# Performance work log

Hardware: AMD Instinct MI355X
Metric: run time of the kernel (lower is better)

Reference implementation:

```python
import jax, jax.numpy as jnp
import numpy as np

TREE = 128
BASIC = 128
EPS = 1e-5


def layer_norm(x, g, b):
    m = jnp.mean(x, axis=-1, keepdims=True)
    v = jnp.mean((x - m) ** 2, axis=-1, keepdims=True)
    return (x - m) * jax.lax.rsqrt(v + EPS) * g + b


def setup_inputs() -> dict:
    key = jax.random.key(0)
    ks = jax.random.split(key, 32)
    n2, n1, n0 = 320000, 80000, 20000
    inp = {
        'subtree_h_top': jax.random.normal(ks[0], (n2, TREE), jnp.float32),
        'atom_x_1': jax.random.normal(ks[1], (n1, BASIC), jnp.float32),
        'atom_x_0': jax.random.normal(ks[2], (n0, BASIC), jnp.float32),
        'bond_x_2': jax.random.normal(ks[3], (n2, BASIC), jnp.float32),
        'bond_x_1': jax.random.normal(ks[4], (n1, BASIC), jnp.float32),
        'branch_W1': jax.random.normal(ks[5], (2, TREE + BASIC, TREE), jnp.float32) * 0.05,
        'branch_b1': jnp.zeros((2, TREE), jnp.float32),
        'branch_g1': jnp.ones((2, TREE), jnp.float32),
        'branch_beta1': jnp.zeros((2, TREE), jnp.float32),
        'branch_W2': jax.random.normal(ks[6], (2, TREE, TREE), jnp.float32) * 0.05,
        'branch_b2': jnp.zeros((2, TREE), jnp.float32),
        'branch_g2': jnp.ones((2, TREE), jnp.float32),
        'branch_beta2': jnp.zeros((2, TREE), jnp.float32),
        'sub_W1': jax.random.normal(ks[7], (2, BASIC + TREE, TREE), jnp.float32) * 0.05,
        'sub_b1': jnp.zeros((2, TREE), jnp.float32),
        'sub_g1': jnp.ones((2, TREE), jnp.float32),
        'sub_beta1': jnp.zeros((2, TREE), jnp.float32),
        'sub_W2': jax.random.normal(ks[8], (2, TREE, TREE), jnp.float32) * 0.05,
        'sub_b2': jnp.zeros((2, TREE), jnp.float32),
        'sub_g2': jnp.ones((2, TREE), jnp.float32),
        'sub_beta2': jnp.zeros((2, TREE), jnp.float32),
        'head_W': jax.random.normal(ks[9], (2, BASIC + TREE, TREE), jnp.float32) * 0.05,
        'head_b': jnp.zeros((2, TREE), jnp.float32),
        'head_g': jnp.ones((2, TREE), jnp.float32),
        'head_beta': jnp.zeros((2, TREE), jnp.float32),
        'src_2': jax.random.randint(ks[10], (n2,), 0, n2),
        'dst_2': jax.random.randint(ks[11], (n2,), 0, n1),
        'src_1': jax.random.randint(ks[12], (n1,), 0, n1),
        'dst_1': jax.random.randint(ks[13], (n1,), 0, n0),
    }
    return inp


def reference(subtree_h_top, atom_x_1, atom_x_0, bond_x_2, bond_x_1,
              branch_W1, branch_b1, branch_g1, branch_beta1,
              branch_W2, branch_b2, branch_g2, branch_beta2,
              sub_W1, sub_b1, sub_g1, sub_beta1,
              sub_W2, sub_b2, sub_g2, sub_beta2,
              head_W, head_b, head_g, head_beta,
              src_2, dst_2, src_1, dst_1):
    relu = jax.nn.relu
    h = subtree_h_top  # subtree_h of level tree_level nodes
    atom_xs = (atom_x_1, atom_x_0)
    bond_xs = (bond_x_2, bond_x_1)
    srcs = (src_2, src_1)
    dsts = (dst_2, dst_1)
    for i in range(2):  # i=0 -> k=2, i=1 -> k=1 (fixed small loop over tree levels)
        ax = atom_xs[i]
        # Branch_Update: edge MLP on [subtree_h[src], bond_x]
        ex = jnp.concatenate([h[srcs[i]], bond_xs[i]], axis=-1)  # [E, tree+basic]
        bh = relu(layer_norm(ex @ branch_W1[i] + branch_b1[i], branch_g1[i], branch_beta1[i]))
        bh = relu(layer_norm(bh @ branch_W2[i] + branch_b2[i], branch_g2[i], branch_beta2[i]))
        # fn.sum aggregation per destination (head) node
        agg = jax.ops.segment_sum(bh, dsts[i], num_segments=ax.shape[0])
        # Tree_Update_Sep
        sx = jnp.concatenate([ax, agg], axis=-1)  # [N, basic+tree]
        f = relu(layer_norm(sx @ sub_W1[i] + sub_b1[i], sub_g1[i], sub_beta1[i]))
        f = relu(layer_norm(f @ sub_W2[i] + sub_b2[i], sub_g2[i], sub_beta2[i]))
        th = jnp.concatenate([ax, f], axis=-1)
        h = relu(layer_norm(th @ head_W[i] + head_b[i], head_g[i], head_beta[i]))
    return h  # subtree_h of atom_0 nodes: [n0, tree_dim]
```

## Files before the change

kernel.cpp:

```cpp
#include <hip/hip_runtime.h>


#define D   128
#define TE  32
#define XS  264

typedef float  f32x4 __attribute__((ext_vector_type(4)));
typedef _Float16 f16x8 __attribute__((ext_vector_type(8)));

__device__ __forceinline__ unsigned short f2h(float f) {
    union { _Float16 h; unsigned short u; } x;
    x.h = (_Float16)f;
    return x.u;
}

__global__ __launch_bounds__(256) void pack_w(
    const float* __restrict__ brW1, const float* __restrict__ brW2,
    const float* __restrict__ sW1,  const float* __restrict__ sW2,
    const float* __restrict__ hW,   unsigned short* __restrict__ Wp)
{
    int p = blockIdx.x * 256 + threadIdx.x;
    const float* src; int off, K;
    if (p < 65536)       { src = brW1; off = 0;      K = 256; }
    else if (p < 98304)  { src = brW2; off = 65536;  K = 128; }
    else if (p < 163840) { src = sW1;  off = 98304;  K = 256; }
    else if (p < 196608) { src = sW2;  off = 163840; K = 128; }
    else                 { src = hW;   off = 196608; K = 256; }
    int q = p - off, lvl, r;
    if (K == 256) { lvl = q >> 15; r = q & 32767; }
    else          { lvl = q >> 14; r = q & 16383; }
    int kb = r >> 12, n = (r >> 5) & 127, kk = r & 31;
    Wp[p] = f2h(src[(size_t)lvl * K * 128 + (size_t)(kb * 32 + kk) * 128 + n]);
}

template<int KB>
__device__ __forceinline__ void gemm_f16(const unsigned short* s_in, int stride,
    const unsigned short* __restrict__ Wp, int rb, int cb, int n15, int q, f32x4 acc[4])
{
    f32x4 zero = {0.f, 0.f, 0.f, 0.f};
#pragma unroll
    for (int ct = 0; ct < 4; ++ct) acc[ct] = zero;
#pragma unroll
    for (int kb = 0; kb < KB; ++kb) {
        f16x8 af = *(const f16x8*)(s_in + (rb + n15) * stride + kb * 32 + q * 8);
        const unsigned short* wb = Wp + (size_t)kb * 4096 + q * 8;
#pragma unroll
        for (int ct = 0; ct < 4; ++ct) {
            f16x8 bf = *(const f16x8*)(wb + (cb + ct * 16 + n15) * 32);
            acc[ct] = __builtin_amdgcn_mfma_f32_16x16x32_f16(af, bf, acc[ct], 0, 0, 0);
        }
    }
}

__device__ __forceinline__ void ln_relu(f32x4 acc[4],
    const float* __restrict__ b, const float* __restrict__ g, const float* __restrict__ be,
    float* s_red, float* s_ms, int rb, int cb, int n15, int q, int wcol, int t)
{
#pragma unroll
    for (int ct = 0; ct < 4; ++ct) {
        float bb = b[cb + ct * 16 + n15];
#pragma unroll
        for (int r = 0; r < 4; ++r) acc[ct][r] += bb;
    }
    float sum[4], ss[4];
#pragma unroll
    for (int r = 0; r < 4; ++r) {
        sum[r] = acc[0][r] + acc[1][r] + acc[2][r] + acc[3][r];
        ss[r]  = acc[0][r]*acc[0][r] + acc[1][r]*acc[1][r]
               + acc[2][r]*acc[2][r] + acc[3][r]*acc[3][r];
    }
#pragma unroll
    for (int off = 1; off < 16; off <<= 1) {
#pragma unroll
        for (int r = 0; r < 4; ++r) {
            sum[r] += __shfl_xor(sum[r], off, 64);
            ss[r]  += __shfl_xor(ss[r],  off, 64);
        }
    }
    if (n15 == 0) {
#pragma unroll
        for (int r = 0; r < 4; ++r) {
            int row = rb + q * 4 + r;
            s_red[row * 4 + wcol * 2 + 0] = sum[r];
            s_red[row * 4 + wcol * 2 + 1] = ss[r];
        }
    }
    __syncthreads();
    if (t < TE) {
        float sm = s_red[t * 4 + 0] + s_red[t * 4 + 2];
        float sq = s_red[t * 4 + 1] + s_red[t * 4 + 3];
        float mean = sm * (1.f / 128.f);
        float var  = sq * (1.f / 128.f) - mean * mean;
        s_ms[t * 2 + 0] = mean;
        s_ms[t * 2 + 1] = rsqrtf(var + 1e-5f);
    }
    __syncthreads();
#pragma unroll
    for (int ct = 0; ct < 4; ++ct) {
        float gg = g[cb + ct * 16 + n15], bb = be[cb + ct * 16 + n15];
#pragma unroll
        for (int r = 0; r < 4; ++r) {
            int row = rb + q * 4 + r;
            float v = (acc[ct][r] - s_ms[row * 2 + 0]) * s_ms[row * 2 + 1] * gg + bb;
            acc[ct][r] = fmaxf(v, 0.f);
        }
    }
}

template<bool HBF16>
__global__ __launch_bounds__(256, 8) void edge_mlp(
    const void* __restrict__ hsrc, const float* __restrict__ bond,
    const int* __restrict__ src, const int* __restrict__ dst,
    const unsigned short* __restrict__ Wp1, const unsigned short* __restrict__ Wp2,
    const float* __restrict__ b1, const float* __restrict__ g1, const float* __restrict__ be1,
    const float* __restrict__ b2, const float* __restrict__ g2, const float* __restrict__ be2,
    float* __restrict__ agg, int E)
{
    __shared__ unsigned short s_x[TE * XS];
    __shared__ float s_red[TE * 4];
    __shared__ float s_ms[TE * 2];
    __shared__ int s_src[TE], s_dst[TE];
    unsigned short* s_y = s_x + 128;

    int t = threadIdx.x, eb = blockIdx.x * TE;
    if (t < TE) {
        int ge = eb + t;
        s_src[t] = (ge < E) ? src[ge] : -1;
        s_dst[t] = (ge < E) ? dst[ge] : -1;
    }
    __syncthreads();

    if (HBF16) {
        const unsigned short* hp = (const unsigned short*)hsrc;
        for (int c = t; c < TE * 16; c += 256) {
            int row = c >> 4, k8 = c & 15;
            int s = s_src[row];
            uint4 v = make_uint4(0, 0, 0, 0);
            if (s >= 0) v = *(const uint4*)(hp + (size_t)s * 128 + k8 * 8);
            *(uint4*)(s_x + row * XS + k8 * 8) = v;
        }
    } else {
        const float* hp = (const float*)hsrc;
        for (int c = t; c < TE * 32; c += 256) {
            int row = c >> 5, k4 = c & 31;
            int s = s_src[row];
            float4 v = make_float4(0, 0, 0, 0);
            if (s >= 0) v = *(const float4*)(hp + (size_t)s * 128 + k4 * 4);
            ushort4 o; o.x = f2h(v.x); o.y = f2h(v.y); o.z = f2h(v.z); o.w = f2h(v.w);
            *(ushort4*)(s_x + row * XS + k4 * 4) = o;
        }
    }
    for (int c = t; c < TE * 32; c += 256) {
        int row = c >> 5, k4 = c & 31;
        int ge = eb + row;
        float4 v = make_float4(0, 0, 0, 0);
        if (ge < E) v = *(const float4*)(bond + (size_t)ge * 128 + k4 * 4);
        ushort4 o; o.x = f2h(v.x); o.y = f2h(v.y); o.z = f2h(v.z); o.w = f2h(v.w);
        *(ushort4*)(s_x + row * XS + 128 + k4 * 4) = o;
    }
    __syncthreads();

    int l = t & 63, w = t >> 6;
    int n15 = l & 15, q = l >> 4;
    int rb = (w & 1) * 16, cb = (w >> 1) * 64, wcol = w >> 1;

    f32x4 acc[4];
    gemm_f16<8>(s_x, XS, Wp1, rb, cb, n15, q, acc);
    ln_relu(acc, b1, g1, be1, s_red, s_ms, rb, cb, n15, q, wcol, t);
#pragma unroll
    for (int ct = 0; ct < 4; ++ct)
#pragma unroll
        for (int r = 0; r < 4; ++r)
            s_y[(rb + q * 4 + r) * XS + cb + ct * 16 + n15] = f2h(acc[ct][r]);
    __syncthreads();
    gemm_f16<4>(s_y, XS, Wp2, rb, cb, n15, q, acc);
    ln_relu(acc, b2, g2, be2, s_red, s_ms, rb, cb, n15, q, wcol, t);

#pragma unroll
    for (int ct = 0; ct < 4; ++ct)
#pragma unroll
        for (int r = 0; r < 4; ++r) {
            int row = rb + q * 4 + r;
            int gd = s_dst[row];
            if (gd >= 0)
                atomicAdd(agg + (size_t)gd * D + cb + ct * 16 + n15, acc[ct][r]);
        }
}

template<bool OUT_F16>
__global__ __launch_bounds__(256, 8) void node_mlp(
    const float* __restrict__ ax, const float* __restrict__ agg,
    const unsigned short* __restrict__ Wp1, const unsigned short* __restrict__ Wp2,
    const unsigned short* __restrict__ Wp3,
    const float* __restrict__ b1, const float* __restrict__ g1, const float* __restrict__ be1,
    const float* __restrict__ b2, const float* __restrict__ g2, const float* __restrict__ be2,
    const float* __restrict__ b3, const float* __restrict__ g3, const float* __restrict__ be3,
    void* __restrict__ out, int N)
{
    __shared__ unsigned short s_x[TE * XS];
    __shared__ float s_red[TE * 4];
    __shared__ float s_ms[TE * 2];
    unsigned short* s_y = s_x + 128;

    int t = threadIdx.x, nb = blockIdx.x * TE;

    for (int c = t; c < TE * 32; c += 256) {
        int row = c >> 5, k4 = c & 31;
        int gr = nb + row;
        float4 v = make_float4(0, 0, 0, 0);
        if (gr < N) v = *(const float4*)(ax + (size_t)gr * 128 + k4 * 4);
        ushort4 o; o.x = f2h(v.x); o.y = f2h(v.y); o.z = f2h(v.z); o.w = f2h(v.w);
        *(ushort4*)(s_x + row * XS + k4 * 4) = o;
    }
    for (int c = t; c < TE * 32; c += 256) {
        int row = c >> 5, k4 = c & 31;
        int gr = nb + row;
        float4 v = make_float4(0, 0, 0, 0);
        if (gr < N) v = *(const float4*)(agg + (size_t)gr * 128 + k4 * 4);
        ushort4 o; o.x = f2h(v.x); o.y = f2h(v.y); o.z = f2h(v.z); o.w = f2h(v.w);
        *(ushort4*)(s_x + row * XS + 128 + k4 * 4) = o;
    }
    __syncthreads();

    int l = t & 63, w = t >> 6;
    int n15 = l & 15, q = l >> 4;
    int rb = (w & 1) * 16, cb = (w >> 1) * 64, wcol = w >> 1;

    f32x4 acc[4];
    gemm_f16<8>(s_x, XS, Wp1, rb, cb, n15, q, acc);
    ln_relu(acc, b1, g1, be1, s_red, s_ms, rb, cb, n15, q, wcol, t);
#pragma unroll
    for (int ct = 0; ct < 4; ++ct)
#pragma unroll
        for (int r = 0; r < 4; ++r)
            s_y[(rb + q * 4 + r) * XS + cb + ct * 16 + n15] = f2h(acc[ct][r]);
    __syncthreads();
    gemm_f16<4>(s_y, XS, Wp2, rb, cb, n15, q, acc);
    ln_relu(acc, b2, g2, be2, s_red, s_ms, rb, cb, n15, q, wcol, t);
#pragma unroll
    for (int ct = 0; ct < 4; ++ct)
#pragma unroll
        for (int r = 0; r < 4; ++r)
            s_x[(rb + q * 4 + r) * XS + 128 + cb + ct * 16 + n15] = f2h(acc[ct][r]);
    __syncthreads();
    gemm_f16<8>(s_x, XS, Wp3, rb, cb, n15, q, acc);
    ln_relu(acc, b3, g3, be3, s_red, s_ms, rb, cb, n15, q, wcol, t);

#pragma unroll
    for (int ct = 0; ct < 4; ++ct)
#pragma unroll
        for (int r = 0; r < 4; ++r) {
            int row = rb + q * 4 + r;
            int gr = nb + row;
            int col = cb + ct * 16 + n15;
            if (gr < N) {
                if (OUT_F16)
                    ((unsigned short*)out)[(size_t)gr * D + col] = f2h(acc[ct][r]);
                else
                    ((float*)out)[(size_t)gr * D + col] = acc[ct][r];
            }
        }
}

extern "C" void kernel_launch(void* const* d_in, const int* in_sizes, int n_in,
                              void* d_out, int out_size, void* d_ws, size_t ws_size,
                              hipStream_t stream)
{
    const float* h2   = (const float*)d_in[0];
    const float* ax1  = (const float*)d_in[1];
    const float* ax0  = (const float*)d_in[2];
    const float* bx2  = (const float*)d_in[3];
    const float* bx1  = (const float*)d_in[4];
    const float* brW1 = (const float*)d_in[5];
    const float* brb1 = (const float*)d_in[6];
    const float* brg1 = (const float*)d_in[7];
    const float* brbe1= (const float*)d_in[8];
    const float* brW2 = (const float*)d_in[9];
    const float* brb2 = (const float*)d_in[10];
    const float* brg2 = (const float*)d_in[11];
    const float* brbe2= (const float*)d_in[12];
    const float* sW1  = (const float*)d_in[13];
    const float* sb1  = (const float*)d_in[14];
    const float* sg1  = (const float*)d_in[15];
    const float* sbe1 = (const float*)d_in[16];
    const float* sW2  = (const float*)d_in[17];
    const float* sb2  = (const float*)d_in[18];
    const float* sg2  = (const float*)d_in[19];
    const float* sbe2 = (const float*)d_in[20];
    const float* hW   = (const float*)d_in[21];
    const float* hb   = (const float*)d_in[22];
    const float* hg   = (const float*)d_in[23];
    const float* hbe  = (const float*)d_in[24];
    const int*   src2 = (const int*)d_in[25];
    const int*   dst2 = (const int*)d_in[26];
    const int*   src1 = (const int*)d_in[27];
    const int*   dst1 = (const int*)d_in[28];

    int n2 = in_sizes[0] / D;
    int n1 = in_sizes[1] / D;
    int n0 = in_sizes[2] / D;

    unsigned short* Wp  = (unsigned short*)d_ws;
    float*          agg = (float*)((char*)d_ws + 524288);
    unsigned short* h1  = (unsigned short*)(agg + (size_t)n1 * D);

    const unsigned short* pBr1[2] = { Wp + 0,      Wp + 32768 };
    const unsigned short* pBr2[2] = { Wp + 65536,  Wp + 65536  + 16384 };
    const unsigned short* pS1 [2] = { Wp + 98304,  Wp + 98304  + 32768 };
    const unsigned short* pS2 [2] = { Wp + 163840, Wp + 163840 + 16384 };
    const unsigned short* pH  [2] = { Wp + 196608, Wp + 196608 + 32768 };

    pack_w<<<dim3(1024), dim3(256), 0, stream>>>(brW1, brW2, sW1, sW2, hW, Wp);

    hipMemsetAsync(agg, 0, (size_t)n1 * D * sizeof(float), stream);
    edge_mlp<false><<<dim3((n2 + TE - 1) / TE), dim3(256), 0, stream>>>(
        h2, bx2, src2, dst2, pBr1[0], pBr2[0],
        brb1, brg1, brbe1, brb2, brg2, brbe2, agg, n2);
    node_mlp<true><<<dim3((n1 + TE - 1) / TE), dim3(256), 0, stream>>>(
        ax1, agg, pS1[0], pS2[0], pH[0],
        sb1, sg1, sbe1, sb2, sg2, sbe2, hb, hg, hbe, h1, n1);

    hipMemsetAsync(agg, 0, (size_t)n0 * D * sizeof(float), stream);
    edge_mlp<true><<<dim3((n1 + TE - 1) / TE), dim3(256), 0, stream>>>(
        h1, bx1, src1, dst1, pBr1[1], pBr2[1],
        brb1 + D, brg1 + D, brbe1 + D, brb2 + D, brg2 + D, brbe2 + D, agg, n1);
    node_mlp<false><<<dim3((n0 + TE - 1) / TE), dim3(256), 0, stream>>>(
        ax0, agg, pS1[1], pS2[1], pH[1],
        sb1 + D, sg1 + D, sbe1 + D, sb2 + D, sg2 + D, sbe2 + D,
        hb + D, hg + D, hbe + D, d_out, n0);
}
```

Baseline: 746.6 us.

## Replace atomic scatter-add aggregation with CSR-sorted edge buffer and segmented gather-sum

Builds a CSR ordering of edges by destination (histogram, three-pass scan, position assignment) for both tree levels up front. The edge MLP now writes its f16 per-edge outputs into a destination-sorted buffer, and the node MLP sums each node's contiguous edge range in registers. This replaces the per-element float atomicAdd scatter into agg and the memset of agg. In exchange it adds several small preprocessing kernels, an extra f16 write and read of the edge outputs, and sums in f16 storage precision. It falls back to the old path if the workspace is too small.

After: 715.7 us. 4.1% less time.

```diff
diff --git a/kernel.cpp b/kernel.cpp
--- a/kernel.cpp
+++ b/kernel.cpp
@@ -33,6 +33,86 @@
     Wp[p] = f2h(src[(size_t)lvl * K * 128 + (size_t)(kb * 32 + kk) * 128 + n]);
 }
 
+
+__global__ __launch_bounds__(256) void csr_hist(
+    const int* __restrict__ dA, int EA, const int* __restrict__ dB, int EB,
+    int* __restrict__ cnt, int AOFFv)
+{
+    int i = blockIdx.x * 256 + threadIdx.x;
+    if (i < EA)               atomicAdd(cnt + dA[i], 1);
+    else if (i - EA < EB)     atomicAdd(cnt + AOFFv + dB[i - EA], 1);
+}
+
+__global__ __launch_bounds__(256) void csr_scanA(
+    const int* __restrict__ cnt, int* __restrict__ inc, int* __restrict__ bsum,
+    int nbA, int AOFFv)
+{
+    __shared__ int lds[256];
+    int b = blockIdx.x, t = threadIdx.x;
+    int lb, ebase, bs;
+    if (b < nbA) { lb = b;       ebase = 0;     bs = lb; }
+    else         { lb = b - nbA; ebase = AOFFv; bs = 128 + lb; }
+    int idx = ebase + lb * 1024 + t * 4;
+    int s0 = cnt[idx], s1 = cnt[idx + 1], s2 = cnt[idx + 2], s3 = cnt[idx + 3];
+    int p1 = s0 + s1, p2 = p1 + s2, p3 = p2 + s3;
+    lds[t] = p3; __syncthreads();
+#pragma unroll
+    for (int o = 1; o < 256; o <<= 1) {
+        int v = (t >= o) ? lds[t - o] : 0;
+        __syncthreads();
+        lds[t] += v;
+        __syncthreads();
+    }
+    int ex = lds[t] - p3;
+    inc[idx] = ex + s0; inc[idx + 1] = ex + p1; inc[idx + 2] = ex + p2; inc[idx + 3] = ex + p3;
+    if (t == 255) bsum[bs] = lds[255];
+}
+
+__global__ __launch_bounds__(256) void csr_scanB(int* __restrict__ bsum, int nbA, int nbB)
+{
+    __shared__ int lds[256];
+    int t = threadIdx.x, seg = t >> 7, i = t & 127;
+    int n = seg ? nbB : nbA;
+    lds[t] = (i < n) ? bsum[t] : 0;
+    __syncthreads();
+#pragma unroll
+    for (int o = 1; o < 128; o <<= 1) {
+        int v = (i >= o) ? lds[t - o] : 0;
+        __syncthreads();
+        lds[t] += v;
+        __syncthreads();
+    }
+    if (i < n) bsum[t] = lds[t];
+}
+
+__global__ __launch_bounds__(256) void csr_scanC(
+    const int* __restrict__ cnt, int* __restrict__ inc, const int* __restrict__ bsum,
+    int* __restrict__ cursor, int nbA, int AOFFv)
+{
+    int b = blockIdx.x, t = threadIdx.x;
+    int lb, ebase, bs;
+    if (b < nbA) { lb = b;       ebase = 0;     bs = lb; }
+    else         { lb = b - nbA; ebase = AOFFv; bs = 128 + lb; }
+    int carry = (lb > 0) ? bsum[bs - 1] : 0;
+    int idx = ebase + lb * 1024 + t * 4;
+#pragma unroll
+    for (int j = 0; j < 4; ++j) {
+        int v = inc[idx + j] + carry;
+        inc[idx + j] = v;
+        cursor[idx + j] = v - cnt[idx + j];
+    }
+}
+
+__global__ __launch_bounds__(256) void csr_pos(
+    const int* __restrict__ dA, int EA, const int* __restrict__ dB, int EB,
+    int* __restrict__ cursor, int* __restrict__ posA, int* __restrict__ posB, int AOFFv)
+{
+    int i = blockIdx.x * 256 + threadIdx.x;
+    if (i < EA)           posA[i] = atomicAdd(cursor + dA[i], 1);
+    else if (i - EA < EB) posB[i - EA] = atomicAdd(cursor + AOFFv + dB[i - EA], 1);
+}
+
+
 template<int KB>
 __device__ __forceinline__ void gemm_f16(const unsigned short* s_in, int stride,
     const unsigned short* __restrict__ Wp, int rb, int cb, int n15, int q, f32x4 acc[4])
@@ -107,26 +187,26 @@
     }
 }
 
-template<bool HBF16>
+template<bool HBF16, bool CSR>
 __global__ __launch_bounds__(256, 8) void edge_mlp(
     const void* __restrict__ hsrc, const float* __restrict__ bond,
-    const int* __restrict__ src, const int* __restrict__ dst,
+    const int* __restrict__ src, const int* __restrict__ dstpos,
     const unsigned short* __restrict__ Wp1, const unsigned short* __restrict__ Wp2,
     const float* __restrict__ b1, const float* __restrict__ g1, const float* __restrict__ be1,
     const float* __restrict__ b2, const float* __restrict__ g2, const float* __restrict__ be2,
-    float* __restrict__ agg, int E)
+    float* __restrict__ agg, unsigned short* __restrict__ ebh, int E)
 {
     __shared__ unsigned short s_x[TE * XS];
     __shared__ float s_red[TE * 4];
     __shared__ float s_ms[TE * 2];
-    __shared__ int s_src[TE], s_dst[TE];
+    __shared__ int s_src[TE], s_idx[TE];
     unsigned short* s_y = s_x + 128;
 
     int t = threadIdx.x, eb = blockIdx.x * TE;
     if (t < TE) {
         int ge = eb + t;
         s_src[t] = (ge < E) ? src[ge] : -1;
-        s_dst[t] = (ge < E) ? dst[ge] : -1;
+        s_idx[t] = (ge < E) ? dstpos[ge] : -1;
     }
     __syncthreads();
 
@@ -176,20 +256,37 @@
     gemm_f16<4>(s_y, XS, Wp2, rb, cb, n15, q, acc);
     ln_relu(acc, b2, g2, be2, s_red, s_ms, rb, cb, n15, q, wcol, t);
 
-#pragma unroll
-    for (int ct = 0; ct < 4; ++ct)
-#pragma unroll
-        for (int r = 0; r < 4; ++r) {
-            int row = rb + q * 4 + r;
-            int gd = s_dst[row];
-            if (gd >= 0)
-                atomicAdd(agg + (size_t)gd * D + cb + ct * 16 + n15, acc[ct][r]);
-        }
-}
-
-template<bool OUT_F16>
+    if (CSR) {
+#pragma unroll
+        for (int ct = 0; ct < 4; ++ct)
+#pragma unroll
+            for (int r = 0; r < 4; ++r)
+                s_x[(rb + q * 4 + r) * XS + cb + ct * 16 + n15] = f2h(acc[ct][r]);
+        __syncthreads();
+        for (int c = t; c < TE * 16; c += 256) {
+            int row = c >> 4, k8 = c & 15;
+            int p = s_idx[row];
+            if (p >= 0)
+                *(uint4*)(ebh + (size_t)p * 128 + k8 * 8) =
+                    *(const uint4*)(s_x + row * XS + k8 * 8);
+        }
+    } else {
+#pragma unroll
+        for (int ct = 0; ct < 4; ++ct)
+#pragma unroll
+            for (int r = 0; r < 4; ++r) {
+                int row = rb + q * 4 + r;
+                int gd = s_idx[row];
+                if (gd >= 0)
+                    atomicAdd(agg + (size_t)gd * D + cb + ct * 16 + n15, acc[ct][r]);
+            }
+    }
+}
+
+template<bool OUT_F16, bool CSR>
 __global__ __launch_bounds__(256, 8) void node_mlp(
     const float* __restrict__ ax, const float* __restrict__ agg,
+    const int* __restrict__ inc, const unsigned short* __restrict__ ebh,
     const unsigned short* __restrict__ Wp1, const unsigned short* __restrict__ Wp2,
     const unsigned short* __restrict__ Wp3,
     const float* __restrict__ b1, const float* __restrict__ g1, const float* __restrict__ be1,
@@ -200,9 +297,16 @@
     __shared__ unsigned short s_x[TE * XS];
     __shared__ float s_red[TE * 4];
     __shared__ float s_ms[TE * 2];
+    __shared__ int s_beg[TE], s_end[TE];
     unsigned short* s_y = s_x + 128;
 
     int t = threadIdx.x, nb = blockIdx.x * TE;
+
+    if (CSR && t < TE) {
+        int gr = nb + t, b0 = 0, e0 = 0;
+        if (gr < N) { e0 = inc[gr]; b0 = (gr == 0) ? 0 : inc[gr - 1]; }
+        s_beg[t] = b0; s_end[t] = e0;
+    }
 
     for (int c = t; c < TE * 32; c += 256) {
         int row = c >> 5, k4 = c & 31;
@@ -212,13 +316,36 @@
         ushort4 o; o.x = f2h(v.x); o.y = f2h(v.y); o.z = f2h(v.z); o.w = f2h(v.w);
         *(ushort4*)(s_x + row * XS + k4 * 4) = o;
     }
-    for (int c = t; c < TE * 32; c += 256) {
-        int row = c >> 5, k4 = c & 31;
-        int gr = nb + row;
-        float4 v = make_float4(0, 0, 0, 0);
-        if (gr < N) v = *(const float4*)(agg + (size_t)gr * 128 + k4 * 4);
-        ushort4 o; o.x = f2h(v.x); o.y = f2h(v.y); o.z = f2h(v.z); o.w = f2h(v.w);
-        *(ushort4*)(s_x + row * XS + 128 + k4 * 4) = o;
+
+    if (CSR) {
+        __syncthreads();
+        int r = t >> 3, s8 = t & 7;
+        float a[16];
+#pragma unroll
+        for (int k = 0; k < 16; ++k) a[k] = 0.f;
+        int jb = s_beg[r], je = s_end[r];
+        for (int j = jb; j < je; ++j) {
+            const unsigned short* rp = ebh + (size_t)j * 128 + s8 * 16;
+            f16x8 v0 = *(const f16x8*)rp;
+            f16x8 v1 = *(const f16x8*)(rp + 8);
+#pragma unroll
+            for (int k = 0; k < 8; ++k) { a[k] += (float)v0[k]; a[8 + k] += (float)v1[k]; }
+        }
+        f16x8 h0, h1;
+#pragma unroll
+        for (int k = 0; k < 8; ++k) { h0[k] = (_Float16)a[k]; h1[k] = (_Float16)a[8 + k]; }
+        unsigned short* op = s_x + r * XS + 128 + s8 * 16;
+        *(f16x8*)op = h0;
+        *(f16x8*)(op + 8) = h1;
+    } else {
+        for (int c = t; c < TE * 32; c += 256) {
+            int row = c >> 5, k4 = c & 31;
+            int gr = nb + row;
+            float4 v = make_float4(0, 0, 0, 0);
+            if (gr < N) v = *(const float4*)(agg + (size_t)gr * 128 + k4 * 4);
+            ushort4 o; o.x = f2h(v.x); o.y = f2h(v.y); o.z = f2h(v.z); o.w = f2h(v.w);
+            *(ushort4*)(s_x + row * XS + 128 + k4 * 4) = o;
+        }
     }
     __syncthreads();
 
@@ -300,9 +427,7 @@
     int n1 = in_sizes[1] / D;
     int n0 = in_sizes[2] / D;
 
-    unsigned short* Wp  = (unsigned short*)d_ws;
-    float*          agg = (float*)((char*)d_ws + 524288);
-    unsigned short* h1  = (unsigned short*)(agg + (size_t)n1 * D);
+    unsigned short* Wp = (unsigned short*)d_ws;
 
     const unsigned short* pBr1[2] = { Wp + 0,      Wp + 32768 };
     const unsigned short* pBr2[2] = { Wp + 65536,  Wp + 65536  + 16384 };
@@ -310,22 +435,74 @@
     const unsigned short* pS2 [2] = { Wp + 163840, Wp + 163840 + 16384 };
     const unsigned short* pH  [2] = { Wp + 196608, Wp + 196608 + 32768 };
 
+    int nbA = (n1 + 1023) / 1024, nbB = (n0 + 1023) / 1024;
+    int AOFFv = nbA * 1024;
+    size_t AN = (size_t)AOFFv + (size_t)nbB * 1024;
+    auto al = [](size_t x) { return (x + 255) & ~(size_t)255; };
+    size_t o = 524288;
+    size_t cnt_o  = o; o = al(o + AN * 4);
+    size_t inc_o  = o; o = al(o + AN * 4);
+    size_t cur_o  = o; o = al(o + AN * 4);
+    size_t bsum_o = o; o = al(o + 1024);
+    size_t posA_o = o; o = al(o + (size_t)n2 * 4);
+    size_t posB_o = o; o = al(o + (size_t)n1 * 4);
+    size_t h1_o   = o; o = al(o + (size_t)n1 * 256);
+    size_t ebh_o  = o; o = al(o + (size_t)n2 * 256);
+    bool use_csr = (ws_size >= o) && (nbA <= 128) && (nbB <= 128);
+
     pack_w<<<dim3(1024), dim3(256), 0, stream>>>(brW1, brW2, sW1, sW2, hW, Wp);
 
-    hipMemsetAsync(agg, 0, (size_t)n1 * D * sizeof(float), stream);
-    edge_mlp<false><<<dim3((n2 + TE - 1) / TE), dim3(256), 0, stream>>>(
-        h2, bx2, src2, dst2, pBr1[0], pBr2[0],
-        brb1, brg1, brbe1, brb2, brg2, brbe2, agg, n2);
-    node_mlp<true><<<dim3((n1 + TE - 1) / TE), dim3(256), 0, stream>>>(
-        ax1, agg, pS1[0], pS2[0], pH[0],
-        sb1, sg1, sbe1, sb2, sg2, sbe2, hb, hg, hbe, h1, n1);
-
-    hipMemsetAsync(agg, 0, (size_t)n0 * D * sizeof(float), stream);
-    edge_mlp<true><<<dim3((n1 + TE - 1) / TE), dim3(256), 0, stream>>>(
-        h1, bx1, src1, dst1, pBr1[1], pBr2[1],
-        brb1 + D, brg1 + D, brbe1 + D, brb2 + D, brg2 + D, brbe2 + D, agg, n1);
-    node_mlp<false><<<dim3((n0 + TE - 1) / TE), dim3(256), 0, stream>>>(
-        ax0, agg, pS1[1], pS2[1], pH[1],
-        sb1 + D, sg1 + D, sbe1 + D, sb2 + D, sg2 + D, sbe2 + D,
-        hb + D, hg + D, hbe + D, d_out, n0);
-}
+    if (use_csr) {
+        int*            cnt    = (int*)((char*)d_ws + cnt_o);
+        int*            inc    = (int*)((char*)d_ws + inc_o);
+        int*            cursor = (int*)((char*)d_ws + cur_o);
+        int*            bsum   = (int*)((char*)d_ws + bsum_o);
+        int*            posA   = (int*)((char*)d_ws + posA_o);
+        int*            posB   = (int*)((char*)d_ws + posB_o);
+        unsigned short* h1     = (unsigned short*)((char*)d_ws + h1_o);
+        unsigned short* ebh    = (unsigned short*)((char*)d_ws + ebh_o);
+
+        int EG = (n2 + n1 + 255) / 256;
+        hipMemsetAsync(cnt, 0, AN * 4, stream);
+        csr_hist <<<dim3(EG),        dim3(256), 0, stream>>>(dst2, n2, dst1, n1, cnt, AOFFv);
+        csr_scanA<<<dim3(nbA + nbB), dim3(256), 0, stream>>>(cnt, inc, bsum, nbA, AOFFv);
+        csr_scanB<<<dim3(1),         dim3(256), 0, stream>>>(bsum, nbA, nbB);
+        csr_scanC<<<dim3(nbA + nbB), dim3(256), 0, stream>>>(cnt, inc, bsum, cursor, nbA, AOFFv);
+        csr_pos  <<<dim3(EG),        dim3(256), 0, stream>>>(dst2, n2, dst1, n1, cursor, posA, posB, AOFFv);
+
+        edge_mlp<false, true><<<dim3((n2 + TE - 1) / TE), dim3(256), 0, stream>>>(
+            h2, bx2, src2, posA, pBr1[0], pBr2[0],
+            brb1, brg1, brbe1, brb2, brg2, brbe2, nullptr, ebh, n2);
+        node_mlp<true, true><<<dim3((n1 + TE - 1) / TE), dim3(256), 0, stream>>>(
+            ax1, nullptr, inc, ebh, pS1[0], pS2[0], pH[0],
+            sb1, sg1, sbe1, sb2, sg2, sbe2, hb, hg, hbe, h1, n1);
+
+        edge_mlp<true, true><<<dim3((n1 + TE - 1) / TE), dim3(256), 0, stream>>>(
+            h1, bx1, src1, posB, pBr1[1], pBr2[1],
+            brb1 + D, brg1 + D, brbe1 + D, brb2 + D, brg2 + D, brbe2 + D, nullptr, ebh, n1);
+        node_mlp<false, true><<<dim3((n0 + TE - 1) / TE), dim3(256), 0, stream>>>(
+            ax0, nullptr, inc + AOFFv, ebh, pS1[1], pS2[1], pH[1],
+            sb1 + D, sg1 + D, sbe1 + D, sb2 + D, sg2 + D, sbe2 + D,
+            hb + D, hg + D, hbe + D, d_out, n0);
+    } else {
+        float*          agg = (float*)((char*)d_ws + 524288);
+        unsigned short* h1  = (unsigned short*)(agg + (size_t)n1 * D);
+
+        hipMemsetAsync(agg, 0, (size_t)n1 * D * sizeof(float), stream);
+        edge_mlp<false, false><<<dim3((n2 + TE - 1) / TE), dim3(256), 0, stream>>>(
+            h2, bx2, src2, dst2, pBr1[0], pBr2[0],
+            brb1, brg1, brbe1, brb2, brg2, brbe2, agg, nullptr, n2);
+        node_mlp<true, false><<<dim3((n1 + TE - 1) / TE), dim3(256), 0, stream>>>(
+            ax1, agg, nullptr, nullptr, pS1[0], pS2[0], pH[0],
+            sb1, sg1, sbe1, sb2, sg2, sbe2, hb, hg, hbe, h1, n1);
+
+        hipMemsetAsync(agg, 0, (size_t)n0 * D * sizeof(float), stream);
+        edge_mlp<true, false><<<dim3((n1 + TE - 1) / TE), dim3(256), 0, stream>>>(
+            h1, bx1, src1, dst1, pBr1[1], pBr2[1],
+            brb1 + D, brg1 + D, brbe1 + D, brb2 + D, brg2 + D, brbe2 + D, agg, nullptr, n1);
+        node_mlp<false, false><<<dim3((n0 + TE - 1) / TE), dim3(256), 0, stream>>>(
+            ax0, agg, nullptr, nullptr, pS1[1], pS2[1], pH[1],
+            sb1 + D, sg1 + D, sbe1 + D, sb2 + D, sg2 + D, sbe2 + D,
+            hb + D, hg + D, hbe + D, d_out, n0);
+    }
+}
```
